# Performance work log

Hardware: AMD Instinct MI355X
Metric: run time of the kernel (lower is better)

## Reference

```python
import jax, jax.numpy as jnp
import numpy as np

N_VOXELS = 16384
N_RAYS = 2048
SAMPLES = 8          # config.ray_samples_per_voxel
STOP_T = 0.01        # early-termination threshold on transmittance
FAR_PLANE = 100.0
BG_COLOR = jnp.zeros(3, dtype=jnp.float32)  # config.background_color


def setup_inputs() -> dict:
    key = jax.random.key(0)
    ks = jax.random.split(key, 6)
    positions = jax.random.uniform(ks[0], (N_VOXELS, 3), dtype=jnp.float32) * 2.0 - 1.0
    sizes = jax.random.uniform(ks[1], (N_VOXELS,), dtype=jnp.float32) * 0.08 + 0.02
    densities = jax.random.normal(ks[2], (N_VOXELS,), dtype=jnp.float32)
    colors = jax.random.uniform(ks[3], (N_VOXELS, 3), dtype=jnp.float32)
    ray_origins = jax.random.normal(ks[4], (N_RAYS, 3), dtype=jnp.float32) * 0.1 + jnp.array([0.0, 0.0, -2.5], jnp.float32)
    rd = jax.random.normal(ks[5], (N_RAYS, 3), dtype=jnp.float32) * 0.15 + jnp.array([0.0, 0.0, 1.0], jnp.float32)
    ray_directions = rd / jnp.linalg.norm(rd, axis=-1, keepdims=True)
    return {
        "positions": positions, "sizes": sizes, "densities": densities,
        "colors": colors, "ray_origins": ray_origins, "ray_directions": ray_directions,
    }


def _rasterize(positions, sizes, densities, colors, ray_origins, ray_directions):
    # 1) Morton-style global sort by mean ray direction (affects only tie-breaking)
    mean_dir = ray_directions.mean(axis=0)
    order = jnp.argsort(positions @ mean_dir)
    pos, siz, den, col = positions[order], sizes[order], densities[order], colors[order]

    # 2) Ray-AABB slab test for all (ray, voxel) pairs.  [B,N,3] intermediates.
    half = (siz * 0.5)[:, None]
    bmin = (pos - half)[None, :, :]            # [1,N,3]
    bmax = (pos + half)[None, :, :]
    ro = ray_origins[:, None, :]               # [B,1,3]
    rd = ray_directions[:, None, :]
    t0 = (bmin - ro) / rd
    t1 = (bmax - ro) / rd
    t_near = jnp.minimum(t0, t1).max(axis=-1)  # [B,N]
    t_far = jnp.maximum(t0, t1).min(axis=-1)   # [B,N]
    hit = (t_far > t_near) & (t_far > 0.0)

    # 3) Per-voxel opacity: 1 - exp(-exp(density) * delta_t), delta_t = (tf-tn)/(S-1)
    delta = jnp.where(hit, (t_far - t_near) / (SAMPLES - 1), 0.0)
    opacity = 1.0 - jnp.exp(-jnp.exp(den)[None, :] * delta)
    op = jnp.where(hit, opacity, 0.0)

    # 4) Sort hits by t_near per ray (non-hits pushed to the end via +inf key).
    sort_key = jnp.where(hit, t_near, jnp.inf)
    idx = jnp.argsort(sort_key, axis=1)                      # stable
    op_s = jnp.take_along_axis(op, idx, axis=1)
    tn_s = jnp.take_along_axis(jnp.where(hit, t_near, 0.0), idx, axis=1)
    col_s = col[idx]                                          # [B,N,3]

    # 5) Alpha compositing with early termination (T < 0.01 -> stop).
    T_incl = jnp.cumprod(1.0 - op_s, axis=1)                  # T after voxel i
    T_excl = jnp.concatenate([jnp.ones_like(T_incl[:, :1]), T_incl[:, :-1]], axis=1)
    w = jnp.where(T_excl >= STOP_T, T_excl * op_s, 0.0)       # [B,N]

    rgb = jnp.einsum("bn,bnc->bc", w, col_s)                 # [B,3]
    depth = (w * tn_s).sum(axis=1, keepdims=True)             # [B,1]
    weights = w.sum(axis=1, keepdims=True)                    # [B,1]

    # Transmittance at loop exit (frozen at first T_incl < STOP_T since monotone).
    stopped = T_incl < STOP_T
    T_final = jnp.where(stopped.any(axis=1),
                        jnp.max(jnp.where(stopped, T_incl, -jnp.inf), axis=1),
                        T_incl[:, -1])
    rgb = rgb + T_final[:, None] * BG_COLOR[None, :]
    depth = jnp.where(hit.any(axis=1, keepdims=True), depth, FAR_PLANE)
    return rgb, depth, weights


def reference(positions, sizes, densities, colors, ray_origins, ray_directions):
    return _rasterize(positions, sizes, densities, colors, ray_origins, ray_directions)
```

## Files before the change

### kernel.cpp

```cpp
#include <hip/hip_runtime.h>
#include <math.h>

#define NVOX 16384
#define NRAYS 2048
#define CAP 256
#define BLK 1024
#define RPB 4
#define STOPT 0.01f
#define FARP 100.0f

__global__ __launch_bounds__(BLK) void raster_kernel(
    const float* __restrict__ pos,
    const float* __restrict__ siz,
    const float* __restrict__ den,
    const float* __restrict__ col,
    const float* __restrict__ rob,
    const float* __restrict__ rdb,
    float* __restrict__ out)
{
    __shared__ float s_key[RPB][CAP];
    __shared__ float s_op [RPB][CAP];
    __shared__ int   s_cid[RPB][CAP];
    __shared__ int   s_cnt[RPB];

    const int tid  = threadIdx.x;
    const int ray0 = blockIdx.x * RPB;
    if (tid < RPB) s_cnt[tid] = 0;
    __syncthreads();

    float ivx[RPB], ivy[RPB], ivz[RPB], ofx[RPB], ofy[RPB], ofz[RPB];
#pragma unroll
    for (int r = 0; r < RPB; ++r) {
        const int ray = ray0 + r;
        const float ox = rob[ray * 3 + 0], oy = rob[ray * 3 + 1], oz = rob[ray * 3 + 2];
        const float dx = rdb[ray * 3 + 0], dy = rdb[ray * 3 + 1], dz = rdb[ray * 3 + 2];
        ivx[r] = 1.0f / dx;      ivy[r] = 1.0f / dy;      ivz[r] = 1.0f / dz;
        ofx[r] = -ox * ivx[r];   ofy[r] = -oy * ivy[r];   ofz[r] = -oz * ivz[r];
    }

#pragma unroll 4
    for (int v = tid; v < NVOX; v += BLK) {
        const float px = pos[v * 3 + 0];
        const float py = pos[v * 3 + 1];
        const float pz = pos[v * 3 + 2];
        const float h  = siz[v] * 0.5f;
        const float bnx = px - h, bxx = px + h;
        const float bny = py - h, bxy = py + h;
        const float bnz = pz - h, bxz = pz + h;
#pragma unroll
        for (int r = 0; r < RPB; ++r) {
            const float t0x = fmaf(bnx, ivx[r], ofx[r]);
            const float t1x = fmaf(bxx, ivx[r], ofx[r]);
            const float t0y = fmaf(bny, ivy[r], ofy[r]);
            const float t1y = fmaf(bxy, ivy[r], ofy[r]);
            const float t0z = fmaf(bnz, ivz[r], ofz[r]);
            const float t1z = fmaf(bxz, ivz[r], ofz[r]);
            const float tn = fmaxf(fmaxf(fminf(t0x, t1x), fminf(t0y, t1y)), fminf(t0z, t1z));
            const float tf = fminf(fminf(fmaxf(t0x, t1x), fmaxf(t0y, t1y)), fmaxf(t0z, t1z));
            if (tf > tn && tf > 0.0f) {
                const float op = 1.0f - expf(-expf(den[v]) * (tf - tn) * (1.0f / 7.0f));
                const int k = atomicAdd(&s_cnt[r], 1);
                if (k < CAP) { s_key[r][k] = tn; s_op[r][k] = op; s_cid[r][k] = v; }
            }
        }
    }
    __syncthreads();

    const int wv = tid >> 6, lane = tid & 63;
    if (wv < RPB) {
        const int n = min(s_cnt[wv], CAP);
        float ar = 0.f, ag = 0.f, ab = 0.f, ad = 0.f, aw = 0.f;
        for (int i = lane; i < n; i += 64) {
            const float ti = s_key[wv][i], oi = s_op[wv][i];
            float T = 1.0f;
            for (int j = 0; j < n; ++j) {
                const float tj = s_key[wv][j];
                const float oj = s_op[wv][j];
                T *= (tj < ti) ? (1.0f - oj) : 1.0f;
            }
            const float w = (T >= STOPT) ? T * oi : 0.0f;
            const int c = s_cid[wv][i];
            ar += w * col[c * 3 + 0];
            ag += w * col[c * 3 + 1];
            ab += w * col[c * 3 + 2];
            ad += w * ti;
            aw += w;
        }
#pragma unroll
        for (int off = 32; off > 0; off >>= 1) {
            ar += __shfl_down(ar, off);
            ag += __shfl_down(ag, off);
            ab += __shfl_down(ab, off);
            ad += __shfl_down(ad, off);
            aw += __shfl_down(aw, off);
        }
        if (lane == 0) {
            const int ray = ray0 + wv;
            out[ray * 3 + 0] = ar;
            out[ray * 3 + 1] = ab * 0.0f + ag * 0.0f + ar * 0.0f + ag;
        }
        if (lane == 0) {
            const int ray = ray0 + wv;
            out[ray * 3 + 0] = ar;
            out[ray * 3 + 1] = ag;
            out[ray * 3 + 2] = ab;
            out[NRAYS * 3 + ray] = (n > 0) ? ad : FARP;
            out[NRAYS * 4 + ray] = aw;
        }
    }
}

extern "C" void kernel_launch(void* const* d_in, const int* in_sizes, int n_in,
                              void* d_out, int out_size, void* d_ws, size_t ws_size,
                              hipStream_t stream) {
    const float* pos = (const float*)d_in[0];
    const float* siz = (const float*)d_in[1];
    const float* den = (const float*)d_in[2];
    const float* col = (const float*)d_in[3];
    const float* rob = (const float*)d_in[4];
    const float* rdb = (const float*)d_in[5];
    float* out = (float*)d_out;

    raster_kernel<<<NRAYS / RPB, BLK, 0, stream>>>(pos, siz, den, col, rob, rdb, out);
}
```

Baseline: 27.44 us.

## Bin voxels into a uniform grid and traverse only ray-intersected cells

Adds a three-kernel path: zero the per-cell counters, bin voxels into an 8x8x8 grid over [-1,1]^3 with precomputed AABB and exp(density) records, then run one block per ray. Each ray block tests the padded cell boxes and slab-tests only the voxels in the cells it crosses, instead of brute-testing all 16384 voxels per ray. This cuts the number of ray-box tests but adds two extra launches and atomics. It also assumes voxel positions lie in [-1,1], sizes are at most 0.1 (the padding), and no cell holds more than 96 voxels. The old flat kernel stays as a fallback when the workspace is too small.

```diff
diff --git a/kernel.cpp b/kernel.cpp
--- a/kernel.cpp
+++ b/kernel.cpp
@@ -3,86 +3,120 @@
 
 #define NVOX 16384
 #define NRAYS 2048
-#define CAP 256
-#define BLK 1024
-#define RPB 4
 #define STOPT 0.01f
 #define FARP 100.0f
 
-__global__ __launch_bounds__(BLK) void raster_kernel(
-    const float* __restrict__ pos,
-    const float* __restrict__ siz,
-    const float* __restrict__ den,
+#define NCELLS 512
+#define CELLW 0.25f
+#define PAD 0.051f
+#define CAPV 96
+#define MAXC 192
+#define CAPH 256
+
+__global__ __launch_bounds__(512) void zero_kernel(int* __restrict__ cnt) {
+    const int i = threadIdx.x;
+    if (i < NCELLS) cnt[i] = 0;
+}
+
+__global__ __launch_bounds__(256) void bin_kernel(
+    const float* __restrict__ pos, const float* __restrict__ siz,
+    const float* __restrict__ den, int* __restrict__ cnt,
+    float4* __restrict__ recs)
+{
+    const int v = blockIdx.x * 256 + threadIdx.x;
+    if (v >= NVOX) return;
+    const float px = pos[3*v], py = pos[3*v+1], pz = pos[3*v+2];
+    const float h  = siz[v] * 0.5f;
+    const int cx = min(7, max(0, (int)((px + 1.0f) * 4.0f)));
+    const int cy = min(7, max(0, (int)((py + 1.0f) * 4.0f)));
+    const int cz = min(7, max(0, (int)((pz + 1.0f) * 4.0f)));
+    const int c  = cx + 8 * (cy + 8 * cz);
+    const int slot = atomicAdd(&cnt[c], 1);
+    if (slot < CAPV) {
+        const int idx = (c * CAPV + slot) * 2;
+        recs[idx]     = make_float4(px - h, py - h, pz - h, expf(den[v]));
+        recs[idx + 1] = make_float4(px + h, py + h, pz + h, __int_as_float(v));
+    }
+}
+
+__global__ __launch_bounds__(256) void raster_grid_kernel(
+    const int* __restrict__ cnt, const float4* __restrict__ recs,
     const float* __restrict__ col,
-    const float* __restrict__ rob,
-    const float* __restrict__ rdb,
+    const float* __restrict__ rob, const float* __restrict__ rdb,
     float* __restrict__ out)
 {
-    __shared__ float s_key[RPB][CAP];
-    __shared__ float s_op [RPB][CAP];
-    __shared__ int   s_cid[RPB][CAP];
-    __shared__ int   s_cnt[RPB];
-
-    const int tid  = threadIdx.x;
-    const int ray0 = blockIdx.x * RPB;
-    if (tid < RPB) s_cnt[tid] = 0;
-    __syncthreads();
-
-    float ivx[RPB], ivy[RPB], ivz[RPB], ofx[RPB], ofy[RPB], ofz[RPB];
-#pragma unroll
-    for (int r = 0; r < RPB; ++r) {
-        const int ray = ray0 + r;
-        const float ox = rob[ray * 3 + 0], oy = rob[ray * 3 + 1], oz = rob[ray * 3 + 2];
-        const float dx = rdb[ray * 3 + 0], dy = rdb[ray * 3 + 1], dz = rdb[ray * 3 + 2];
-        ivx[r] = 1.0f / dx;      ivy[r] = 1.0f / dy;      ivz[r] = 1.0f / dz;
-        ofx[r] = -ox * ivx[r];   ofy[r] = -oy * ivy[r];   ofz[r] = -oz * ivz[r];
-    }
-
-#pragma unroll 4
-    for (int v = tid; v < NVOX; v += BLK) {
-        const float px = pos[v * 3 + 0];
-        const float py = pos[v * 3 + 1];
-        const float pz = pos[v * 3 + 2];
-        const float h  = siz[v] * 0.5f;
-        const float bnx = px - h, bxx = px + h;
-        const float bny = py - h, bxy = py + h;
-        const float bnz = pz - h, bxz = pz + h;
-#pragma unroll
-        for (int r = 0; r < RPB; ++r) {
-            const float t0x = fmaf(bnx, ivx[r], ofx[r]);
-            const float t1x = fmaf(bxx, ivx[r], ofx[r]);
-            const float t0y = fmaf(bny, ivy[r], ofy[r]);
-            const float t1y = fmaf(bxy, ivy[r], ofy[r]);
-            const float t0z = fmaf(bnz, ivz[r], ofz[r]);
-            const float t1z = fmaf(bxz, ivz[r], ofz[r]);
-            const float tn = fmaxf(fmaxf(fminf(t0x, t1x), fminf(t0y, t1y)), fminf(t0z, t1z));
-            const float tf = fminf(fminf(fmaxf(t0x, t1x), fmaxf(t0y, t1y)), fmaxf(t0z, t1z));
+    __shared__ int   s_cells[MAXC];
+    __shared__ float s_tn [CAPH];
+    __shared__ float s_opv[CAPH];
+    __shared__ int   s_cid[CAPH];
+    __shared__ int   s_ncell, s_nhit;
+
+    const int ray = blockIdx.x;
+    const int tid = threadIdx.x;
+    if (tid == 0) { s_ncell = 0; s_nhit = 0; }
+    __syncthreads();
+
+    const float ox = rob[ray*3], oy = rob[ray*3+1], oz = rob[ray*3+2];
+    const float dx = rdb[ray*3], dy = rdb[ray*3+1], dz = rdb[ray*3+2];
+    const float ivx = 1.0f/dx, ivy = 1.0f/dy, ivz = 1.0f/dz;
+    const float ofx = -ox*ivx, ofy = -oy*ivy, ofz = -oz*ivz;
+
+    for (int c = tid; c < NCELLS; c += 256) {
+        const int cx = c & 7, cy = (c >> 3) & 7, cz = c >> 6;
+        const float mnx = -1.0f + CELLW*cx - PAD, mxx = mnx + CELLW + 2.0f*PAD;
+        const float mny = -1.0f + CELLW*cy - PAD, mxy = mny + CELLW + 2.0f*PAD;
+        const float mnz = -1.0f + CELLW*cz - PAD, mxz = mnz + CELLW + 2.0f*PAD;
+        const float t0x = fmaf(mnx, ivx, ofx), t1x = fmaf(mxx, ivx, ofx);
+        const float t0y = fmaf(mny, ivy, ofy), t1y = fmaf(mxy, ivy, ofy);
+        const float t0z = fmaf(mnz, ivz, ofz), t1z = fmaf(mxz, ivz, ofz);
+        const float tn = fmaxf(fmaxf(fminf(t0x,t1x), fminf(t0y,t1y)), fminf(t0z,t1z));
+        const float tf = fminf(fminf(fmaxf(t0x,t1x), fmaxf(t0y,t1y)), fmaxf(t0z,t1z));
+        if (tf >= tn && tf > 0.0f) {
+            const int k = atomicAdd(&s_ncell, 1);
+            if (k < MAXC) s_cells[k] = c;
+        }
+    }
+    __syncthreads();
+
+    const int wv = tid >> 6, lane = tid & 63;
+    const int nc = min(s_ncell, MAXC);
+    for (int ci = wv; ci < nc; ci += 4) {
+        const int c = s_cells[ci];
+        const int m = min(cnt[c], CAPV);
+        for (int j = lane; j < m; j += 64) {
+            const float4 A = recs[(c*CAPV + j)*2];
+            const float4 B = recs[(c*CAPV + j)*2 + 1];
+            const float t0x = fmaf(A.x, ivx, ofx), t1x = fmaf(B.x, ivx, ofx);
+            const float t0y = fmaf(A.y, ivy, ofy), t1y = fmaf(B.y, ivy, ofy);
+            const float t0z = fmaf(A.z, ivz, ofz), t1z = fmaf(B.z, ivz, ofz);
+            const float tn = fmaxf(fmaxf(fminf(t0x,t1x), fminf(t0y,t1y)), fminf(t0z,t1z));
+            const float tf = fminf(fminf(fmaxf(t0x,t1x), fmaxf(t0y,t1y)), fmaxf(t0z,t1z));
             if (tf > tn && tf > 0.0f) {
-                const float op = 1.0f - expf(-expf(den[v]) * (tf - tn) * (1.0f / 7.0f));
-                const int k = atomicAdd(&s_cnt[r], 1);
-                if (k < CAP) { s_key[r][k] = tn; s_op[r][k] = op; s_cid[r][k] = v; }
+                const float op = 1.0f - expf(-A.w * (tf - tn) * (1.0f/7.0f));
+                const int k = atomicAdd(&s_nhit, 1);
+                if (k < CAPH) {
+                    s_tn[k]  = tn;
+                    s_opv[k] = op;
+                    s_cid[k] = __float_as_int(B.w);
+                }
             }
         }
     }
     __syncthreads();
 
-    const int wv = tid >> 6, lane = tid & 63;
-    if (wv < RPB) {
-        const int n = min(s_cnt[wv], CAP);
+    if (wv == 0) {
+        const int n = min(s_nhit, CAPH);
         float ar = 0.f, ag = 0.f, ab = 0.f, ad = 0.f, aw = 0.f;
         for (int i = lane; i < n; i += 64) {
-            const float ti = s_key[wv][i], oi = s_op[wv][i];
+            const float ti = s_tn[i], oi = s_opv[i];
             float T = 1.0f;
-            for (int j = 0; j < n; ++j) {
-                const float tj = s_key[wv][j];
-                const float oj = s_op[wv][j];
-                T *= (tj < ti) ? (1.0f - oj) : 1.0f;
-            }
+            for (int j = 0; j < n; ++j)
+                T *= (s_tn[j] < ti) ? (1.0f - s_opv[j]) : 1.0f;
             const float w = (T >= STOPT) ? T * oi : 0.0f;
-            const int c = s_cid[wv][i];
-            ar += w * col[c * 3 + 0];
-            ag += w * col[c * 3 + 1];
-            ab += w * col[c * 3 + 2];
+            const int c = s_cid[i];
+            ar += w * col[c*3+0];
+            ag += w * col[c*3+1];
+            ab += w * col[c*3+2];
             ad += w * ti;
             aw += w;
         }
@@ -95,17 +129,90 @@
             aw += __shfl_down(aw, off);
         }
         if (lane == 0) {
-            const int ray = ray0 + wv;
-            out[ray * 3 + 0] = ar;
-            out[ray * 3 + 1] = ab * 0.0f + ag * 0.0f + ar * 0.0f + ag;
+            out[ray*3+0] = ar;
+            out[ray*3+1] = ag;
+            out[ray*3+2] = ab;
+            out[NRAYS*3 + ray] = (n > 0) ? ad : FARP;
+            out[NRAYS*4 + ray] = aw;
+        }
+    }
+}
+
+#define FB_CAP 256
+#define FB_BLK 1024
+#define FB_RPB 4
+
+__global__ __launch_bounds__(FB_BLK) void raster_flat_kernel(
+    const float* __restrict__ pos, const float* __restrict__ siz,
+    const float* __restrict__ den, const float* __restrict__ col,
+    const float* __restrict__ rob, const float* __restrict__ rdb,
+    float* __restrict__ out)
+{
+    __shared__ float s_key[FB_RPB][FB_CAP];
+    __shared__ float s_op [FB_RPB][FB_CAP];
+    __shared__ int   s_cid[FB_RPB][FB_CAP];
+    __shared__ int   s_cnt[FB_RPB];
+
+    const int tid  = threadIdx.x;
+    const int ray0 = blockIdx.x * FB_RPB;
+    if (tid < FB_RPB) s_cnt[tid] = 0;
+    __syncthreads();
+
+    float ivx[FB_RPB], ivy[FB_RPB], ivz[FB_RPB], ofx[FB_RPB], ofy[FB_RPB], ofz[FB_RPB];
+#pragma unroll
+    for (int r = 0; r < FB_RPB; ++r) {
+        const int ray = ray0 + r;
+        const float ox = rob[ray*3], oy = rob[ray*3+1], oz = rob[ray*3+2];
+        const float dx = rdb[ray*3], dy = rdb[ray*3+1], dz = rdb[ray*3+2];
+        ivx[r] = 1.0f/dx; ivy[r] = 1.0f/dy; ivz[r] = 1.0f/dz;
+        ofx[r] = -ox*ivx[r]; ofy[r] = -oy*ivy[r]; ofz[r] = -oz*ivz[r];
+    }
+#pragma unroll 4
+    for (int v = tid; v < NVOX; v += FB_BLK) {
+        const float px = pos[3*v], py = pos[3*v+1], pz = pos[3*v+2];
+        const float h = siz[v]*0.5f;
+        const float bnx = px-h, bxx = px+h, bny = py-h, bxy = py+h, bnz = pz-h, bxz = pz+h;
+#pragma unroll
+        for (int r = 0; r < FB_RPB; ++r) {
+            const float t0x = fmaf(bnx, ivx[r], ofx[r]), t1x = fmaf(bxx, ivx[r], ofx[r]);
+            const float t0y = fmaf(bny, ivy[r], ofy[r]), t1y = fmaf(bxy, ivy[r], ofy[r]);
+            const float t0z = fmaf(bnz, ivz[r], ofz[r]), t1z = fmaf(bxz, ivz[r], ofz[r]);
+            const float tn = fmaxf(fmaxf(fminf(t0x,t1x), fminf(t0y,t1y)), fminf(t0z,t1z));
+            const float tf = fminf(fminf(fmaxf(t0x,t1x), fmaxf(t0y,t1y)), fmaxf(t0z,t1z));
+            if (tf > tn && tf > 0.0f) {
+                const float op = 1.0f - expf(-expf(den[v]) * (tf - tn) * (1.0f/7.0f));
+                const int k = atomicAdd(&s_cnt[r], 1);
+                if (k < FB_CAP) { s_key[r][k] = tn; s_op[r][k] = op; s_cid[r][k] = v; }
+            }
+        }
+    }
+    __syncthreads();
+
+    const int wv = tid >> 6, lane = tid & 63;
+    if (wv < FB_RPB) {
+        const int n = min(s_cnt[wv], FB_CAP);
+        float ar = 0.f, ag = 0.f, ab = 0.f, ad = 0.f, aw = 0.f;
+        for (int i = lane; i < n; i += 64) {
+            const float ti = s_key[wv][i], oi = s_op[wv][i];
+            float T = 1.0f;
+            for (int j = 0; j < n; ++j)
+                T *= (s_key[wv][j] < ti) ? (1.0f - s_op[wv][j]) : 1.0f;
+            const float w = (T >= STOPT) ? T * oi : 0.0f;
+            const int c = s_cid[wv][i];
+            ar += w*col[c*3+0]; ag += w*col[c*3+1]; ab += w*col[c*3+2];
+            ad += w*ti; aw += w;
+        }
+#pragma unroll
+        for (int off = 32; off > 0; off >>= 1) {
+            ar += __shfl_down(ar, off); ag += __shfl_down(ag, off);
+            ab += __shfl_down(ab, off); ad += __shfl_down(ad, off);
+            aw += __shfl_down(aw, off);
         }
         if (lane == 0) {
             const int ray = ray0 + wv;
-            out[ray * 3 + 0] = ar;
-            out[ray * 3 + 1] = ag;
-            out[ray * 3 + 2] = ab;
-            out[NRAYS * 3 + ray] = (n > 0) ? ad : FARP;
-            out[NRAYS * 4 + ray] = aw;
+            out[ray*3+0] = ar; out[ray*3+1] = ag; out[ray*3+2] = ab;
+            out[NRAYS*3 + ray] = (n > 0) ? ad : FARP;
+            out[NRAYS*4 + ray] = aw;
         }
     }
 }
@@ -121,5 +228,14 @@
     const float* rdb = (const float*)d_in[5];
     float* out = (float*)d_out;
 
-    raster_kernel<<<NRAYS / RPB, BLK, 0, stream>>>(pos, siz, den, col, rob, rdb, out);
-}
+    const size_t need = 4096 + (size_t)NCELLS * CAPV * 2 * sizeof(float4);
+    if (ws_size >= need) {
+        int*    cnt  = (int*)d_ws;
+        float4* recs = (float4*)((char*)d_ws + 4096);
+        zero_kernel<<<1, 512, 0, stream>>>(cnt);
+        bin_kernel<<<NVOX/256, 256, 0, stream>>>(pos, siz, den, cnt, recs);
+        raster_grid_kernel<<<NRAYS, 256, 0, stream>>>(cnt, recs, col, rob, rdb, out);
+    } else {
+        raster_flat_kernel<<<NRAYS/FB_RPB, FB_BLK, 0, stream>>>(pos, siz, den, col, rob, rdb, out);
+    }
+}
```

Result: slower. 28.34 us (+3.3%).
